# Optimization experiments

Measured on AMD Instinct MI355X. Metric: run time of the kernel, lower is better.

Reference implementation:

```python
import jax, jax.numpy as jnp
import numpy as np

D_MODEL = 1024
NUM_HEADS = 16
HEAD_DIM = D_MODEL // NUM_HEADS
B, S = 4, 2048


def setup_inputs() -> dict:
    key = jax.random.key(0)
    ks = jax.random.split(key, 6)
    scale = 1.0 / np.sqrt(D_MODEL)
    return {
        "q": jax.random.normal(ks[0], (B, S, D_MODEL), dtype=jnp.float32),
        "k": jax.random.normal(ks[1], (B, S, D_MODEL), dtype=jnp.float32),
        "v": jax.random.normal(ks[2], (B, S, D_MODEL), dtype=jnp.float32),
        "Wq": jax.random.normal(ks[3], (D_MODEL, D_MODEL), dtype=jnp.float32) * scale,
        "Wk": jax.random.normal(ks[4], (D_MODEL, D_MODEL), dtype=jnp.float32) * scale,
        "Wv": jax.random.normal(ks[5], (D_MODEL, D_MODEL), dtype=jnp.float32) * scale,
    }


def reference(q, k, v, Wq, Wk, Wv):
    b, s, d = q.shape
    # nn.Linear(bias=False): x @ W.T
    qp = jnp.einsum('bsd,ed->bse', q, Wq)
    kp = jnp.einsum('bsd,ed->bse', k, Wk)
    vp = jnp.einsum('bsd,ed->bse', v, Wv)
    # split heads -> (B, H, S, Dh)
    qh = qp.reshape(b, s, NUM_HEADS, HEAD_DIM).transpose(0, 2, 1, 3)
    kh = kp.reshape(b, s, NUM_HEADS, HEAD_DIM).transpose(0, 2, 1, 3)
    vh = vp.reshape(b, s, NUM_HEADS, HEAD_DIM).transpose(0, 2, 1, 3)
    scores = jnp.einsum('bhqd,bhkd->bhqk', qh, kh) / jnp.sqrt(jnp.float32(HEAD_DIM))
    attn = jax.nn.softmax(scores, axis=-1)
    att = jnp.einsum('bhqk,bhkd->bhqd', attn, vh)
    # NOTE: faithful to the source, which does a raw .view (no head transpose back)
    return att.reshape(b, s, d)
```

## Files before the change

kernel.cpp:

```cpp
#include <hip/hip_runtime.h>
#include <hip/hip_bf16.h>
#include <stdint.h>

#define D_MODEL 1024
#define NHEAD   16
#define HDIM    64
#define BATCH   4
#define SEQ     2048
#define NTOK    (BATCH*SEQ)

typedef __bf16          b16x8 __attribute__((ext_vector_type(8)));
typedef unsigned short  u16x8 __attribute__((ext_vector_type(8)));
typedef unsigned short  u16x4 __attribute__((ext_vector_type(4)));
typedef float           f32x4 __attribute__((ext_vector_type(4)));

__device__ __forceinline__ unsigned short f2b(float f) {
  union { float f; uint32_t u; } c; c.f = f;
  return (unsigned short)((c.u + 0x7FFFu + ((c.u >> 16) & 1u)) >> 16);
}

__device__ __forceinline__ uint32_t cvtpk(float lo, float hi) {
  uint32_t r;
  asm("v_cvt_pk_bf16_f32 %0, %1, %2" : "=v"(r) : "v"(lo), "v"(hi));
  return r;
}

__device__ __forceinline__ b16x8 cv8(f32x4 a, f32x4 b) {
  b16x8 r;
#pragma unroll
  for (int i = 0; i < 4; i++) { r[i] = (__bf16)a[i]; r[i + 4] = (__bf16)b[i]; }
  return r;
}

__device__ __forceinline__ void glds16(const void* g, void* l) {
  __builtin_amdgcn_global_load_lds(
      (const __attribute__((address_space(1))) unsigned int*)g,
      (__attribute__((address_space(3))) unsigned int*)l, 16, 0, 0);
}

__global__ __launch_bounds__(256, 8)
void wpack_kernel(const float* __restrict__ Wq, const float* __restrict__ Wk,
                  const float* __restrict__ Wv, unsigned short* __restrict__ wsp) {
  int bid = blockIdx.x;
  int which = bid >> 8;
  int tn = (bid >> 5) & 7;
  int kt = bid & 31;
  const float* W = (which == 0) ? Wq : ((which == 1) ? Wk : Wv);
  int t = threadIdx.x;
  int r = t >> 1;
  int sw0 = (t & 1) * 2;
  char* dst = (char*)wsp + (size_t)bid * 8192 + t * 32;
  const float* src = W + (size_t)(tn * 128 + r) * D_MODEL + kt * 32;
#pragma unroll
  for (int i = 0; i < 2; i++) {
    int s = (sw0 + i) ^ ((r >> 1) & 3);
    f32x4 a = *(const f32x4*)(src + s * 8);
    f32x4 b = *(const f32x4*)(src + s * 8 + 4);
    u16x8 pk;
#pragma unroll
    for (int j = 0; j < 4; j++) { pk[j] = f2b(a[j]); pk[j + 4] = f2b(b[j]); }
    *(u16x8*)(dst + i * 16) = pk;
  }
}

__global__ __launch_bounds__(256, 3)
void proj_gemm_kernel(const float* __restrict__ q, const float* __restrict__ k,
                      const float* __restrict__ v, const unsigned short* __restrict__ wsp,
                      unsigned short* __restrict__ qp, unsigned short* __restrict__ kp,
                      unsigned short* __restrict__ vt) {
  __shared__ __align__(16) char lds[2][24576];

  int bid = blockIdx.x;
  int swz = (bid & 7) * 192 + (bid >> 3);
  int which = swz >> 9;
  int rr = swz & 511;
  int tm = rr >> 3, tn = rr & 7;

  const float* X = (which == 0) ? q : ((which == 1) ? k : v);
  const char* Bpack = (const char*)wsp + (size_t)((which * 8 + tn) * 32) * 8192;

  int tid  = threadIdx.x;
  int lane = tid & 63;
  int w    = tid >> 6;
  int g    = lane >> 4;
  int c    = lane & 15;
  int chi  = c & 7;
  int wr   = (w >> 1) * 64;
  int wc   = (w & 1) * 64;

  f32x4 acc[4][4];
#pragma unroll
  for (int m = 0; m < 4; m++)
#pragma unroll
    for (int n = 0; n < 4; n++) acc[m][n] = (f32x4){0.f, 0.f, 0.f, 0.f};

  int arowl = lane >> 3;
  int aswz  = ((lane & 7) ^ arowl) << 4;
  const char* Asrc = (const char*)(X + (size_t)(tm * 128 + w * 32 + arowl) * D_MODEL) + aswz;
  const char* Bsrc = Bpack + w * 2048 + lane * 16;

  int aoff0 = (wr + c) * 128 + ((2 * g    ^ chi) << 4);
  int aoff1 = (wr + c) * 128 + (((2*g+1) ^ chi) << 4);
  int rboff = 16384 + (wc + c) * 64 + ((g ^ ((c >> 1) & 3)) << 4);

#pragma unroll
  for (int i = 0; i < 4; i++)
    glds16(Asrc + (size_t)i * 8 * D_MODEL * 4, lds[0] + w * 4096 + i * 1024);
  glds16(Bsrc,        lds[0] + 16384 + w * 2048);
  glds16(Bsrc + 1024, lds[0] + 16384 + w * 2048 + 1024);

  for (int kt = 0; kt < 32; kt++) {
    __syncthreads();
    if (kt < 31) {
      char* nb = lds[(kt + 1) & 1];
#pragma unroll
      for (int i = 0; i < 4; i++)
        glds16(Asrc + (size_t)i * 8 * D_MODEL * 4 + (kt + 1) * 128, nb + w * 4096 + i * 1024);
      glds16(Bsrc + (size_t)(kt + 1) * 8192,        nb + 16384 + w * 2048);
      glds16(Bsrc + (size_t)(kt + 1) * 8192 + 1024, nb + 16384 + w * 2048 + 1024);
    }
    const char* buf = lds[kt & 1];
    b16x8 af[4];
    u16x8 bf[4];
#pragma unroll
    for (int m = 0; m < 4; m++) {
      f32x4 a0 = *(const f32x4*)(buf + aoff0 + m * 2048);
      f32x4 a1 = *(const f32x4*)(buf + aoff1 + m * 2048);
      af[m] = cv8(a0, a1);
    }
#pragma unroll
    for (int n = 0; n < 4; n++)
      bf[n] = *(const u16x8*)(buf + rboff + n * 1024);
#pragma unroll
    for (int m = 0; m < 4; m++)
#pragma unroll
      for (int n = 0; n < 4; n++)
        acc[m][n] = __builtin_amdgcn_mfma_f32_16x16x32_bf16(
            af[m], __builtin_bit_cast(b16x8, bf[n]), acc[m][n], 0, 0, 0);
  }

  int cbase = tn * 128 + wc;
  int rbase = tm * 128 + wr;
  if (which < 2) {
    unsigned short* OutP = (which == 0) ? qp : kp;
    float scale = (which == 0) ? 0.18033688f : 1.0f;
#pragma unroll
    for (int m = 0; m < 4; m++)
#pragma unroll
      for (int n = 0; n < 4; n++) {
        int e = cbase + n * 16 + c;
        int h = e >> 6, dh = e & 63;
#pragma unroll
        for (int j = 0; j < 4; j++) {
          int i = rbase + m * 16 + g * 4 + j;
          int b = i >> 11, s = i & 2047;
          OutP[(((size_t)(b * NHEAD + h)) * SEQ + s) * HDIM + dh] =
              f2b(acc[m][n][j] * scale);
        }
      }
  } else {
#pragma unroll
    for (int m = 0; m < 4; m++)
#pragma unroll
      for (int n = 0; n < 4; n++) {
        int e = cbase + n * 16 + c;
        int h = e >> 6, dh = e & 63;
        int i0 = rbase + m * 16 + g * 4;
        int b = i0 >> 11, s0 = i0 & 2047;
        u16x4 pk;
#pragma unroll
        for (int j = 0; j < 4; j++) pk[j] = f2b(acc[m][n][j]);
        *(u16x4*)&vt[(((size_t)(b * NHEAD + h)) * HDIM + dh) * SEQ + s0] = pk;
      }
  }
}

#define KVB 64
__global__ __launch_bounds__(256, 3)
void attn_kernel(const unsigned short* __restrict__ qp,
                 const unsigned short* __restrict__ kp,
                 const unsigned short* __restrict__ vt,
                 float* __restrict__ out) {
  __shared__ __align__(16) char lds[2][16384];

  int bid = blockIdx.x;
  int swz = (bid & 7) * 128 + (bid >> 3);
  int bh = swz >> 4;
  int qb = swz & 15;

  int tid  = threadIdx.x;
  int lane = tid & 63;
  int w    = tid >> 6;
  int g    = lane >> 4;
  int c    = lane & 15;
  int chi  = c & 7;

  const unsigned short* Kg = kp + (size_t)bh * SEQ * HDIM;
  const unsigned short* Vg = vt + (size_t)bh * HDIM * SEQ;

  int q0 = qb * 128 + w * 32;
  u16x8 qf[2][2];
#pragma unroll
  for (int qg = 0; qg < 2; qg++)
#pragma unroll
    for (int h = 0; h < 2; h++)
      qf[qg][h] = *(const u16x8*)&qp[((size_t)bh * SEQ + q0 + qg * 16 + c) * HDIM + h * 32 + g * 8];

  f32x4 o[4][2];
#pragma unroll
  for (int d = 0; d < 4; d++)
#pragma unroll
    for (int qg = 0; qg < 2; qg++) o[d][qg] = (f32x4){0.f, 0.f, 0.f, 0.f};
  float l[2] = {0.f, 0.f};

  int koffA = c * 128 + ((g * 16) ^ (chi << 4));
  int koffB = c * 128 + (((64 + g * 16)) ^ (chi << 4));
  int voff[2][2];
#pragma unroll
  for (int w2 = 0; w2 < 2; w2++) {
    int b0 = w2 * 64 + g * 8;
    voff[w2][0] = 8192 + c * 128 + ((((b0      >> 4) ^ chi) << 4) + (b0 & 15));
    voff[w2][1] = 8192 + c * 128 + (((((b0+32) >> 4) ^ chi) << 4) + (b0 & 15));
  }
  int arow = tid >> 3, aseg = tid & 7;
  int kwo = arow * 128 + ((aseg * 16) ^ ((arow & 7) << 4));
  int vwo = 8192 + kwo;

  char* cur = lds[0];
  char* nxt = lds[1];

  u16x8 kreg[2], vreg[2];
  kreg[0] = *(const u16x8*)&Kg[(size_t)arow * HDIM + aseg * 8];
  kreg[1] = *(const u16x8*)&Kg[(size_t)(arow + 32) * HDIM + aseg * 8];
  vreg[0] = *(const u16x8*)&Vg[(size_t)arow * SEQ + aseg * 8];
  vreg[1] = *(const u16x8*)&Vg[(size_t)(arow + 32) * SEQ + aseg * 8];
  *(u16x8*)(cur + kwo)        = kreg[0];
  *(u16x8*)(cur + kwo + 4096) = kreg[1];
  *(u16x8*)(cur + vwo)        = vreg[0];
  *(u16x8*)(cur + vwo + 4096) = vreg[1];
  __syncthreads();

  for (int t = 0; t < SEQ / KVB; t++) {
    if (t < SEQ / KVB - 1) {
      int kv1 = (t + 1) * KVB;
      kreg[0] = *(const u16x8*)&Kg[(size_t)(kv1 + arow) * HDIM + aseg * 8];
      kreg[1] = *(const u16x8*)&Kg[(size_t)(kv1 + arow + 32) * HDIM + aseg * 8];
      vreg[0] = *(const u16x8*)&Vg[(size_t)arow * SEQ + kv1 + aseg * 8];
      vreg[1] = *(const u16x8*)&Vg[(size_t)(arow + 32) * SEQ + kv1 + aseg * 8];
    }

    f32x4 sf[4][2];
#pragma unroll
    for (int st = 0; st < 4; st++) {
      u16x8 kf0 = *(const u16x8*)(cur + koffA + st * 2048);
      u16x8 kf1 = *(const u16x8*)(cur + koffB + st * 2048);
#pragma unroll
      for (int qg = 0; qg < 2; qg++) {
        sf[st][qg] = __builtin_amdgcn_mfma_f32_16x16x32_bf16(
            __builtin_bit_cast(b16x8, kf0), __builtin_bit_cast(b16x8, qf[qg][0]),
            (f32x4){0.f, 0.f, 0.f, 0.f}, 0, 0, 0);
        sf[st][qg] = __builtin_amdgcn_mfma_f32_16x16x32_bf16(
            __builtin_bit_cast(b16x8, kf1), __builtin_bit_cast(b16x8, qf[qg][1]),
            sf[st][qg], 0, 0, 0);
      }
    }

    union { uint32_t u[4]; u16x8 v; } pb[2][2];
#pragma unroll
    for (int qg = 0; qg < 2; qg++) {
      float p[4][4];
#pragma unroll
      for (int st = 0; st < 4; st++)
#pragma unroll
        for (int j = 0; j < 4; j++) p[st][j] = exp2f(sf[st][qg][j]);
      float s01 = ((p[0][0] + p[0][1]) + (p[0][2] + p[0][3])) +
                  ((p[1][0] + p[1][1]) + (p[1][2] + p[1][3]));
      float s23 = ((p[2][0] + p[2][1]) + (p[2][2] + p[2][3])) +
                  ((p[3][0] + p[3][1]) + (p[3][2] + p[3][3]));
      l[qg] += s01 + s23;
#pragma unroll
      for (int w2 = 0; w2 < 2; w2++) {
        pb[w2][qg].u[0] = cvtpk(p[2*w2][0],   p[2*w2][1]);
        pb[w2][qg].u[1] = cvtpk(p[2*w2][2],   p[2*w2][3]);
        pb[w2][qg].u[2] = cvtpk(p[2*w2+1][0], p[2*w2+1][1]);
        pb[w2][qg].u[3] = cvtpk(p[2*w2+1][2], p[2*w2+1][3]);
      }
    }

#pragma unroll
    for (int w2 = 0; w2 < 2; w2++)
#pragma unroll
      for (int d = 0; d < 4; d++) {
        union { u16x4 h[2]; u16x8 v; } afu;
        afu.h[0] = *(const u16x4*)(cur + voff[w2][0] + d * 2048);
        afu.h[1] = *(const u16x4*)(cur + voff[w2][1] + d * 2048);
#pragma unroll
        for (int qg = 0; qg < 2; qg++)
          o[d][qg] = __builtin_amdgcn_mfma_f32_16x16x32_bf16(
              __builtin_bit_cast(b16x8, afu.v), __builtin_bit_cast(b16x8, pb[w2][qg].v),
              o[d][qg], 0, 0, 0);
      }

    if (t < SEQ / KVB - 1) {
      *(u16x8*)(nxt + kwo)        = kreg[0];
      *(u16x8*)(nxt + kwo + 4096) = kreg[1];
      *(u16x8*)(nxt + vwo)        = vreg[0];
      *(u16x8*)(nxt + vwo + 4096) = vreg[1];
    }
    __syncthreads();
    char* tmp = cur; cur = nxt; nxt = tmp;
  }

#pragma unroll
  for (int qg = 0; qg < 2; qg++) {
    l[qg] += __shfl_xor(l[qg], 16);
    l[qg] += __shfl_xor(l[qg], 32);
  }
#pragma unroll
  for (int qg = 0; qg < 2; qg++) {
    float inv = 1.f / l[qg];
    float* orow = out + ((size_t)bh * SEQ + q0 + qg * 16 + c) * HDIM;
#pragma unroll
    for (int d = 0; d < 4; d++) {
      f32x4 val;
#pragma unroll
      for (int j = 0; j < 4; j++) val[j] = o[d][qg][j] * inv;
      *(f32x4*)(orow + d * 16 + g * 4) = val;
    }
  }
}

extern "C" void kernel_launch(void* const* d_in, const int* in_sizes, int n_in,
                              void* d_out, int out_size, void* d_ws, size_t ws_size,
                              hipStream_t stream) {
  const float* q  = (const float*)d_in[0];
  const float* k  = (const float*)d_in[1];
  const float* v  = (const float*)d_in[2];
  const float* Wq = (const float*)d_in[3];
  const float* Wk = (const float*)d_in[4];
  const float* Wv = (const float*)d_in[5];

  unsigned short* qp  = (unsigned short*)d_ws;
  unsigned short* kp  = qp + (size_t)NTOK * D_MODEL;
  unsigned short* vt  = kp + (size_t)NTOK * D_MODEL;
  unsigned short* wsp = vt + (size_t)NTOK * D_MODEL;
  float* out = (float*)d_out;

  hipLaunchKernelGGL(wpack_kernel, dim3(768), dim3(256), 0, stream,
                     Wq, Wk, Wv, wsp);
  hipLaunchKernelGGL(proj_gemm_kernel, dim3(1536), dim3(256), 0, stream,
                     q, k, v, wsp, qp, kp, vt);
  hipLaunchKernelGGL(attn_kernel, dim3(1024), dim3(256), 0, stream,
                     qp, kp, vt, out);
}
```

Baseline: 180.1 us.

## Pre-pack activations to swizzled bf16 tiles and use pure-bf16 projection GEMM

```diff
diff --git a/kernel.cpp b/kernel.cpp
--- a/kernel.cpp
+++ b/kernel.cpp
@@ -37,6 +37,7 @@
       (const __attribute__((address_space(1))) unsigned int*)g,
       (__attribute__((address_space(3))) unsigned int*)l, 16, 0, 0);
 }
+
 
 __global__ __launch_bounds__(256, 8)
 void wpack_kernel(const float* __restrict__ Wq, const float* __restrict__ Wk,
@@ -63,11 +64,148 @@
   }
 }
 
+__global__ __launch_bounds__(256, 8)
+void xpack_kernel(const float* __restrict__ q, const float* __restrict__ k,
+                  const float* __restrict__ v, unsigned short* __restrict__ xsp) {
+  int bid = blockIdx.x;
+  int which = bid >> 11;
+  int tm = (bid >> 5) & 63;
+  int kt = bid & 31;
+  const float* X = (which == 0) ? q : ((which == 1) ? k : v);
+  int t = threadIdx.x;
+  int r = t >> 1;
+  int sw0 = (t & 1) * 2;
+  char* dst = (char*)xsp + (size_t)bid * 8192 + t * 32;
+  const float* src = X + (size_t)(tm * 128 + r) * D_MODEL + kt * 32;
+#pragma unroll
+  for (int i = 0; i < 2; i++) {
+    int s = (sw0 + i) ^ ((r >> 1) & 3);
+    f32x4 a = *(const f32x4*)(src + s * 8);
+    f32x4 b = *(const f32x4*)(src + s * 8 + 4);
+    u16x8 pk;
+#pragma unroll
+    for (int j = 0; j < 4; j++) { pk[j] = f2b(a[j]); pk[j + 4] = f2b(b[j]); }
+    *(u16x8*)(dst + i * 16) = pk;
+  }
+}
+
+__device__ __forceinline__ void proj_epilogue(
+    int which, int tm, int tn, int g, int c, f32x4 (&acc)[4][4],
+    unsigned short* qp, unsigned short* kp, unsigned short* vt) {
+  int cbase = tn * 128 + (0);
+  (void)cbase;
+}
+
+__global__ __launch_bounds__(256, 4)
+void proj_gemm_bf16(const unsigned short* __restrict__ xsp,
+                    const unsigned short* __restrict__ wsp,
+                    unsigned short* __restrict__ qp, unsigned short* __restrict__ kp,
+                    unsigned short* __restrict__ vt) {
+  __shared__ __align__(16) char lds[2][16384];
+
+  int bid = blockIdx.x;
+  int swz = (bid & 7) * 192 + (bid >> 3);
+  int which = swz >> 9;
+  int rr = swz & 511;
+  int tm = rr >> 3, tn = rr & 7;
+
+  const char* Apack = (const char*)xsp + (size_t)(((which << 6) + tm) * 32) * 8192;
+  const char* Bpack = (const char*)wsp + (size_t)(((which << 3) + tn) * 32) * 8192;
+
+  int tid  = threadIdx.x;
+  int lane = tid & 63;
+  int w    = tid >> 6;
+  int g    = lane >> 4;
+  int c    = lane & 15;
+  int wr   = (w >> 1) * 64;
+  int wc   = (w & 1) * 64;
+
+  f32x4 acc[4][4];
+#pragma unroll
+  for (int m = 0; m < 4; m++)
+#pragma unroll
+    for (int n = 0; n < 4; n++) acc[m][n] = (f32x4){0.f, 0.f, 0.f, 0.f};
+
+  const char* Asrc = Apack + w * 2048 + lane * 16;
+  const char* Bsrc = Bpack + w * 2048 + lane * 16;
+
+  int rco   = ((g ^ ((c >> 1) & 3)) << 4);
+  int raoff = (wr + c) * 64 + rco;
+  int rboff = 8192 + (wc + c) * 64 + rco;
+
+  glds16(Asrc,        lds[0] + w * 2048);
+  glds16(Asrc + 1024, lds[0] + w * 2048 + 1024);
+  glds16(Bsrc,        lds[0] + 8192 + w * 2048);
+  glds16(Bsrc + 1024, lds[0] + 8192 + w * 2048 + 1024);
+
+  for (int kt = 0; kt < 32; kt++) {
+    __syncthreads();
+    if (kt < 31) {
+      char* nb = lds[(kt + 1) & 1];
+      size_t off = (size_t)(kt + 1) * 8192;
+      glds16(Asrc + off,        nb + w * 2048);
+      glds16(Asrc + off + 1024, nb + w * 2048 + 1024);
+      glds16(Bsrc + off,        nb + 8192 + w * 2048);
+      glds16(Bsrc + off + 1024, nb + 8192 + w * 2048 + 1024);
+    }
+    const char* buf = lds[kt & 1];
+    u16x8 af[4], bf[4];
+#pragma unroll
+    for (int m = 0; m < 4; m++)
+      af[m] = *(const u16x8*)(buf + raoff + m * 1024);
+#pragma unroll
+    for (int n = 0; n < 4; n++)
+      bf[n] = *(const u16x8*)(buf + rboff + n * 1024);
+#pragma unroll
+    for (int m = 0; m < 4; m++)
+#pragma unroll
+      for (int n = 0; n < 4; n++)
+        acc[m][n] = __builtin_amdgcn_mfma_f32_16x16x32_bf16(
+            __builtin_bit_cast(b16x8, af[m]), __builtin_bit_cast(b16x8, bf[n]),
+            acc[m][n], 0, 0, 0);
+  }
+
+  int cbase = tn * 128 + wc;
+  int rbase = tm * 128 + wr;
+  if (which < 2) {
+    unsigned short* OutP = (which == 0) ? qp : kp;
+    float scale = (which == 0) ? 0.18033688f : 1.0f;
+#pragma unroll
+    for (int m = 0; m < 4; m++)
+#pragma unroll
+      for (int n = 0; n < 4; n++) {
+        int e = cbase + n * 16 + c;
+        int h = e >> 6, dh = e & 63;
+#pragma unroll
+        for (int j = 0; j < 4; j++) {
+          int i = rbase + m * 16 + g * 4 + j;
+          int b = i >> 11, s = i & 2047;
+          OutP[(((size_t)(b * NHEAD + h)) * SEQ + s) * HDIM + dh] =
+              f2b(acc[m][n][j] * scale);
+        }
+      }
+  } else {
+#pragma unroll
+    for (int m = 0; m < 4; m++)
+#pragma unroll
+      for (int n = 0; n < 4; n++) {
+        int e = cbase + n * 16 + c;
+        int h = e >> 6, dh = e & 63;
+        int i0 = rbase + m * 16 + g * 4;
+        int b = i0 >> 11, s0 = i0 & 2047;
+        u16x4 pk;
+#pragma unroll
+        for (int j = 0; j < 4; j++) pk[j] = f2b(acc[m][n][j]);
+        *(u16x4*)&vt[(((size_t)(b * NHEAD + h)) * HDIM + dh) * SEQ + s0] = pk;
+      }
+  }
+}
+
 __global__ __launch_bounds__(256, 3)
-void proj_gemm_kernel(const float* __restrict__ q, const float* __restrict__ k,
-                      const float* __restrict__ v, const unsigned short* __restrict__ wsp,
-                      unsigned short* __restrict__ qp, unsigned short* __restrict__ kp,
-                      unsigned short* __restrict__ vt) {
+void proj_gemm_f32a(const float* __restrict__ q, const float* __restrict__ k,
+                    const float* __restrict__ v, const unsigned short* __restrict__ wsp,
+                    unsigned short* __restrict__ qp, unsigned short* __restrict__ kp,
+                    unsigned short* __restrict__ vt) {
   __shared__ __align__(16) char lds[2][24576];
 
   int bid = blockIdx.x;
@@ -340,16 +478,27 @@
   const float* Wk = (const float*)d_in[4];
   const float* Wv = (const float*)d_in[5];
 
+  const size_t projBytes = (size_t)NTOK * D_MODEL * 2;
   unsigned short* qp  = (unsigned short*)d_ws;
-  unsigned short* kp  = qp + (size_t)NTOK * D_MODEL;
-  unsigned short* vt  = kp + (size_t)NTOK * D_MODEL;
-  unsigned short* wsp = vt + (size_t)NTOK * D_MODEL;
+  unsigned short* kp  = (unsigned short*)((char*)d_ws + projBytes);
+  unsigned short* vt  = (unsigned short*)((char*)d_ws + 2 * projBytes);
+  unsigned short* wsp = (unsigned short*)((char*)d_ws + 3 * projBytes);
+  const size_t wspBytes = (size_t)768 * 8192;
+  unsigned short* xsp = (unsigned short*)((char*)d_ws + 3 * projBytes + wspBytes);
+  const size_t need = 3 * projBytes + wspBytes + (size_t)6144 * 8192;
   float* out = (float*)d_out;
 
   hipLaunchKernelGGL(wpack_kernel, dim3(768), dim3(256), 0, stream,
                      Wq, Wk, Wv, wsp);
-  hipLaunchKernelGGL(proj_gemm_kernel, dim3(1536), dim3(256), 0, stream,
-                     q, k, v, wsp, qp, kp, vt);
+  if (ws_size >= need) {
+    hipLaunchKernelGGL(xpack_kernel, dim3(6144), dim3(256), 0, stream,
+                       q, k, v, xsp);
+    hipLaunchKernelGGL(proj_gemm_bf16, dim3(1536), dim3(256), 0, stream,
+                       xsp, wsp, qp, kp, vt);
+  } else {
+    hipLaunchKernelGGL(proj_gemm_f32a, dim3(1536), dim3(256), 0, stream,
+                       q, k, v, wsp, qp, kp, vt);
+  }
   hipLaunchKernelGGL(attn_kernel, dim3(1024), dim3(256), 0, stream,
                      qp, kp, vt, out);
 }
```

New measurement: 198.3 us. 10.1% more time.

## Compute softmax row sums via MFMA with ones; add wave priority hints

Applied to the files above, without the earlier changes.

```diff
diff --git a/kernel.cpp b/kernel.cpp
--- a/kernel.cpp
+++ b/kernel.cpp
@@ -64,10 +64,10 @@
 }
 
 __global__ __launch_bounds__(256, 3)
-void proj_gemm_kernel(const float* __restrict__ q, const float* __restrict__ k,
-                      const float* __restrict__ v, const unsigned short* __restrict__ wsp,
-                      unsigned short* __restrict__ qp, unsigned short* __restrict__ kp,
-                      unsigned short* __restrict__ vt) {
+void proj_gemm_f32a(const float* __restrict__ q, const float* __restrict__ k,
+                    const float* __restrict__ v, const unsigned short* __restrict__ wsp,
+                    unsigned short* __restrict__ qp, unsigned short* __restrict__ kp,
+                    unsigned short* __restrict__ vt) {
   __shared__ __align__(16) char lds[2][24576];
 
   int bid = blockIdx.x;
@@ -211,7 +211,11 @@
   for (int d = 0; d < 4; d++)
 #pragma unroll
     for (int qg = 0; qg < 2; qg++) o[d][qg] = (f32x4){0.f, 0.f, 0.f, 0.f};
-  float l[2] = {0.f, 0.f};
+  f32x4 lacc[2];
+  lacc[0] = (f32x4){0.f, 0.f, 0.f, 0.f};
+  lacc[1] = (f32x4){0.f, 0.f, 0.f, 0.f};
+
+  const u16x8 ones = {0x3F80, 0x3F80, 0x3F80, 0x3F80, 0x3F80, 0x3F80, 0x3F80, 0x3F80};
 
   int koffA = c * 128 + ((g * 16) ^ (chi << 4));
   int koffB = c * 128 + (((64 + g * 16)) ^ (chi << 4));
@@ -229,11 +233,14 @@
   char* cur = lds[0];
   char* nxt = lds[1];
 
+  const unsigned short* KgP = Kg + (size_t)arow * HDIM + aseg * 8;
+  const unsigned short* VgP = Vg + (size_t)arow * SEQ + aseg * 8;
+
   u16x8 kreg[2], vreg[2];
-  kreg[0] = *(const u16x8*)&Kg[(size_t)arow * HDIM + aseg * 8];
-  kreg[1] = *(const u16x8*)&Kg[(size_t)(arow + 32) * HDIM + aseg * 8];
-  vreg[0] = *(const u16x8*)&Vg[(size_t)arow * SEQ + aseg * 8];
-  vreg[1] = *(const u16x8*)&Vg[(size_t)(arow + 32) * SEQ + aseg * 8];
+  kreg[0] = *(const u16x8*)(KgP);
+  kreg[1] = *(const u16x8*)(KgP + 32 * HDIM);
+  vreg[0] = *(const u16x8*)(VgP);
+  vreg[1] = *(const u16x8*)(VgP + 32 * SEQ);
   *(u16x8*)(cur + kwo)        = kreg[0];
   *(u16x8*)(cur + kwo + 4096) = kreg[1];
   *(u16x8*)(cur + vwo)        = vreg[0];
@@ -242,14 +249,16 @@
 
   for (int t = 0; t < SEQ / KVB; t++) {
     if (t < SEQ / KVB - 1) {
-      int kv1 = (t + 1) * KVB;
-      kreg[0] = *(const u16x8*)&Kg[(size_t)(kv1 + arow) * HDIM + aseg * 8];
-      kreg[1] = *(const u16x8*)&Kg[(size_t)(kv1 + arow + 32) * HDIM + aseg * 8];
-      vreg[0] = *(const u16x8*)&Vg[(size_t)arow * SEQ + kv1 + aseg * 8];
-      vreg[1] = *(const u16x8*)&Vg[(size_t)(arow + 32) * SEQ + kv1 + aseg * 8];
+      KgP += KVB * HDIM;
+      VgP += KVB;
+      kreg[0] = *(const u16x8*)(KgP);
+      kreg[1] = *(const u16x8*)(KgP + 32 * HDIM);
+      vreg[0] = *(const u16x8*)(VgP);
+      vreg[1] = *(const u16x8*)(VgP + 32 * SEQ);
     }
 
     f32x4 sf[4][2];
+    __builtin_amdgcn_s_setprio(1);
 #pragma unroll
     for (int st = 0; st < 4; st++) {
       u16x8 kf0 = *(const u16x8*)(cur + koffA + st * 2048);
@@ -264,6 +273,7 @@
             sf[st][qg], 0, 0, 0);
       }
     }
+    __builtin_amdgcn_s_setprio(0);
 
     union { uint32_t u[4]; u16x8 v; } pb[2][2];
 #pragma unroll
@@ -273,11 +283,6 @@
       for (int st = 0; st < 4; st++)
 #pragma unroll
         for (int j = 0; j < 4; j++) p[st][j] = exp2f(sf[st][qg][j]);
-      float s01 = ((p[0][0] + p[0][1]) + (p[0][2] + p[0][3])) +
-                  ((p[1][0] + p[1][1]) + (p[1][2] + p[1][3]));
-      float s23 = ((p[2][0] + p[2][1]) + (p[2][2] + p[2][3])) +
-                  ((p[3][0] + p[3][1]) + (p[3][2] + p[3][3]));
-      l[qg] += s01 + s23;
 #pragma unroll
       for (int w2 = 0; w2 < 2; w2++) {
         pb[w2][qg].u[0] = cvtpk(p[2*w2][0],   p[2*w2][1]);
@@ -287,8 +292,9 @@
       }
     }
 
-#pragma unroll
-    for (int w2 = 0; w2 < 2; w2++)
+    __builtin_amdgcn_s_setprio(1);
+#pragma unroll
+    for (int w2 = 0; w2 < 2; w2++) {
 #pragma unroll
       for (int d = 0; d < 4; d++) {
         union { u16x4 h[2]; u16x8 v; } afu;
@@ -300,6 +306,13 @@
               __builtin_bit_cast(b16x8, afu.v), __builtin_bit_cast(b16x8, pb[w2][qg].v),
               o[d][qg], 0, 0, 0);
       }
+#pragma unroll
+      for (int qg = 0; qg < 2; qg++)
+        lacc[qg] = __builtin_amdgcn_mfma_f32_16x16x32_bf16(
+            __builtin_bit_cast(b16x8, ones), __builtin_bit_cast(b16x8, pb[w2][qg].v),
+            lacc[qg], 0, 0, 0);
+    }
+    __builtin_amdgcn_s_setprio(0);
 
     if (t < SEQ / KVB - 1) {
       *(u16x8*)(nxt + kwo)        = kreg[0];
@@ -313,12 +326,7 @@
 
 #pragma unroll
   for (int qg = 0; qg < 2; qg++) {
-    l[qg] += __shfl_xor(l[qg], 16);
-    l[qg] += __shfl_xor(l[qg], 32);
-  }
-#pragma unroll
-  for (int qg = 0; qg < 2; qg++) {
-    float inv = 1.f / l[qg];
+    float inv = 1.f / lacc[qg][0];
     float* orow = out + ((size_t)bh * SEQ + q0 + qg * 16 + c) * HDIM;
 #pragma unroll
     for (int d = 0; d < 4; d++) {
@@ -340,15 +348,16 @@
   const float* Wk = (const float*)d_in[4];
   const float* Wv = (const float*)d_in[5];
 
+  const size_t projBytes = (size_t)NTOK * D_MODEL * 2;
   unsigned short* qp  = (unsigned short*)d_ws;
-  unsigned short* kp  = qp + (size_t)NTOK * D_MODEL;
-  unsigned short* vt  = kp + (size_t)NTOK * D_MODEL;
-  unsigned short* wsp = vt + (size_t)NTOK * D_MODEL;
+  unsigned short* kp  = (unsigned short*)((char*)d_ws + projBytes);
+  unsigned short* vt  = (unsigned short*)((char*)d_ws + 2 * projBytes);
+  unsigned short* wsp = (unsigned short*)((char*)d_ws + 3 * projBytes);
   float* out = (float*)d_out;
 
   hipLaunchKernelGGL(wpack_kernel, dim3(768), dim3(256), 0, stream,
                      Wq, Wk, Wv, wsp);
-  hipLaunchKernelGGL(proj_gemm_kernel, dim3(1536), dim3(256), 0, stream,
+  hipLaunchKernelGGL(proj_gemm_f32a, dim3(1536), dim3(256), 0, stream,
                      q, k, v, wsp, qp, kp, vt);
   hipLaunchKernelGGL(attn_kernel, dim3(1024), dim3(256), 0, stream,
                      qp, kp, vt, out);
```

Result: faster. 175.3 us (-2.6%).
